# Performance work log

Measured on AMD Instinct MI355X. Metric: run time of the kernel, lower is better.

## Reference

```python
import jax, jax.numpy as jnp
import numpy as np

MODEL_DIM = 512
NUM_HEADS = 8
HEAD_DIM = MODEL_DIM // NUM_HEADS  # 64
NUM_NODE = 1024
CLUSTER = 128
S = 60
EMBED = 0.5


def setup_inputs() -> dict:
    key = jax.random.key(0)
    ks = jax.random.split(key, 16)
    d = MODEL_DIM
    sc = 1.0 / np.sqrt(d)
    inp = {
        "x": jax.random.normal(ks[0], (4, 12, NUM_NODE, d), dtype=jnp.float32),
        "Wq": jax.random.normal(ks[1], (d, d), dtype=jnp.float32) * sc,
        "bq": jnp.zeros((d,), jnp.float32),
        "Wk": jax.random.normal(ks[2], (d, d), dtype=jnp.float32) * sc,
        "bk": jnp.zeros((d,), jnp.float32),
        "Wv": jax.random.normal(ks[3], (d, d), dtype=jnp.float32) * sc,
        "bv": jnp.zeros((d,), jnp.float32),
        "We": jax.random.normal(ks[4], (d, d), dtype=jnp.float32) * sc,
        "be": jnp.zeros((d,), jnp.float32),
        "Wo": jax.random.normal(ks[5], (d, d), dtype=jnp.float32) * sc,
        "bo": jnp.zeros((d,), jnp.float32),
        # adp_pos is initialized to zeros in torch; use small randn for a non-degenerate test
        "adp_pos": jax.random.normal(ks[6], (NUM_NODE, CLUSTER), dtype=jnp.float32) * 0.02,
        "U1": jax.random.normal(ks[7], (HEAD_DIM, S), dtype=jnp.float32) * np.sqrt(2.0 / (HEAD_DIM + S)),
        "U2": jax.random.normal(ks[8], (S, HEAD_DIM), dtype=jnp.float32) * np.sqrt(2.0 / (S + HEAD_DIM)),
    }
    return inp


def _split_heads(t):
    # torch.cat(torch.split(t, head_dim, -1), 0): heads stacked head-major on batch dim
    return jnp.concatenate(jnp.split(t, NUM_HEADS, axis=-1), axis=0)


def _merge_heads(t):
    return jnp.concatenate(jnp.split(t, NUM_HEADS, axis=0), axis=-1)


def _pool_nodes(t):
    # AdaptiveAvgPool2d((CLUSTER, None)) on (B,T,N,D) with N % CLUSTER == 0 -> block mean
    B, T, N, D = t.shape
    return t.reshape(B, T, CLUSTER, N // CLUSTER, D).mean(axis=3)


def reference(x, Wq, bq, Wk, bk, Wv, bv, We, be, Wo, bo, adp_pos, U1, U2):
    q = x @ Wq.T + bq                      # (B,T,N,D)
    k = _pool_nodes(x @ Wk.T + bk)          # (B,T,C,D)
    v = _pool_nodes(x @ Wv.T + bv)          # (B,T,C,D)
    ev = x @ We.T + be                      # (B,T,N,D)

    qh = _split_heads(q)                    # (B*H,T,N,d)
    kh = _split_heads(k)                    # (B*H,T,C,d)
    vh = _split_heads(v)                    # (B*H,T,C,d)
    evh = _split_heads(ev)                  # (B*H,T,N,d)

    # external attention branch: softmax over node dim (-2)
    exa = jax.nn.softmax(evh @ U1, axis=-2)  # (B*H,T,N,S)
    exa_val = (exa @ U2) * EMBED + evh       # (B*H,T,N,d)

    score = jnp.einsum("btnd,btcd->btnc", qh, kh) / np.sqrt(HEAD_DIM)
    score = score + adp_pos[None, None]      # (B*H,T,N,C)
    attn = jax.nn.softmax(score, axis=-1)

    out = attn @ vh + exa_val                # (B*H,T,N,d)
    out = _merge_heads(out)                  # (B,T,N,D)
    return out @ Wo.T + bo
```

## Files before the change

### kernel.cpp

```cpp
#include <hip/hip_runtime.h>


#define LOG2E 1.44269504088896f

typedef __attribute__((ext_vector_type(4))) float f32x4;
typedef __attribute__((ext_vector_type(8))) short bf16x8;

__device__ __forceinline__ unsigned short f2bf(float f) {
    union { float f; unsigned u; } v; v.f = f;
    unsigned r = (v.u + 0x7fffu + ((v.u >> 16) & 1u)) >> 16;
    return (unsigned short)r;
}
__device__ __forceinline__ float bf2f(unsigned short h) {
    union { unsigned u; float f; } v; v.u = ((unsigned)h) << 16;
    return v.f;
}

__global__ void cvt_w(const float* __restrict__ Wq, const float* __restrict__ Wk,
                      const float* __restrict__ Wv, const float* __restrict__ We,
                      const float* __restrict__ Wo, const float* __restrict__ U1,
                      const float* __restrict__ U2,
                      const float* __restrict__ bq, const float* __restrict__ bk,
                      const float* __restrict__ bv, const float* __restrict__ be,
                      unsigned short* __restrict__ Wqe, unsigned short* __restrict__ Wkv,
                      unsigned short* __restrict__ Wob, unsigned short* __restrict__ U1T,
                      unsigned short* __restrict__ U2bT,
                      float* __restrict__ bqe, float* __restrict__ bkv)
{
    int i = blockIdx.x * 256 + threadIdx.x;
    if (i < 524288) {
        int r = i >> 9;
        float v = (r < 512) ? Wq[i] : We[i - 262144];
        Wqe[i] = f2bf(v);
    } else if (i < 1048576) {
        int j = i - 524288; int r = j >> 9;
        float v = (r < 512) ? Wk[j] : Wv[j - 262144];
        Wkv[j] = f2bf(v);
    } else if (i < 1310720) {
        int j = i - 1048576;
        Wob[j] = f2bf(Wo[j]);
    } else if (i < 1314816) {
        int j = i - 1310720; int s = j >> 6, k = j & 63;
        U1T[j] = (s < 60) ? f2bf(U1[k * 60 + s]) : (unsigned short)0;
    } else if (i < 1318912) {
        int j = i - 1314816; int d = j >> 6, s = j & 63;
        U2bT[j] = (s < 60) ? f2bf(U2[s * 64 + d] * 0.5f) : (unsigned short)0;
    } else if (i < 1319936) {
        int j = i - 1318912;
        bqe[j] = (j < 512) ? bq[j] : be[j - 512];
    } else if (i < 1320960) {
        int j = i - 1319936;
        bkv[j] = (j < 512) ? bk[j] : bv[j - 512];
    }
}

__global__ void cvt_pool(const float* __restrict__ x, unsigned short* __restrict__ xb,
                         unsigned short* __restrict__ xpb)
{
    int i = blockIdx.x * 256 + threadIdx.x;
    int d4 = i & 127;
    int btc = i >> 7;
    int bt = btc >> 7, c = btc & 127;
    long base = ((long)(bt * 1024 + c * 8)) * 128 + d4;
    const float4* src = (const float4*)x + base;
    ushort4* dst = (ushort4*)xb + base;
    float sx = 0.f, sy = 0.f, sz = 0.f, sw = 0.f;
#pragma unroll
    for (int j = 0; j < 8; j++) {
        float4 v = src[(long)j * 128];
        sx += v.x; sy += v.y; sz += v.z; sw += v.w;
        ushort4 o;
        o.x = f2bf(v.x); o.y = f2bf(v.y); o.z = f2bf(v.z); o.w = f2bf(v.w);
        dst[(long)j * 128] = o;
    }
    ushort4 p;
    p.x = f2bf(sx * 0.125f); p.y = f2bf(sy * 0.125f);
    p.z = f2bf(sz * 0.125f); p.w = f2bf(sw * 0.125f);
    ((ushort4*)xpb)[(long)btc * 128 + d4] = p;
}

template <int OUTF32>
__global__ __launch_bounds__(256, 2) void gemm_bt(
    const unsigned short* __restrict__ A, const unsigned short* __restrict__ W,
    const float* __restrict__ bias, void* __restrict__ Cout,
    int M, int N, int K)
{
    __shared__ __attribute__((aligned(16))) unsigned short As[128 * 32];
    __shared__ __attribute__((aligned(16))) unsigned short Bs[128 * 32];
    const int tid = threadIdx.x;
    const int wave = tid >> 6, lane = tid & 63;
    const int quad = lane >> 4, l16 = lane & 15;
    const int m0 = blockIdx.x * 128, n0 = blockIdx.y * 128;
    const int wm = (wave & 1) * 64, wn = (wave >> 1) * 64;

    f32x4 acc[4][4];
#pragma unroll
    for (int i = 0; i < 4; i++)
#pragma unroll
        for (int j = 0; j < 4; j++) acc[i][j] = (f32x4){0.f, 0.f, 0.f, 0.f};

    const int c0 = tid, c1 = tid + 256;
    const int r0 = c0 >> 2, kc0 = (c0 & 3) * 8;
    const int r1 = c1 >> 2, kc1 = (c1 & 3) * 8;

    for (int k0 = 0; k0 < K; k0 += 32) {
        int4 a0 = *(const int4*)(A + (long)(m0 + r0) * K + k0 + kc0);
        int4 a1 = *(const int4*)(A + (long)(m0 + r1) * K + k0 + kc1);
        int4 b0 = *(const int4*)(W + (long)(n0 + r0) * K + k0 + kc0);
        int4 b1 = *(const int4*)(W + (long)(n0 + r1) * K + k0 + kc1);
        __syncthreads();
        *(int4*)&As[c0 * 8] = a0; *(int4*)&As[c1 * 8] = a1;
        *(int4*)&Bs[c0 * 8] = b0; *(int4*)&Bs[c1 * 8] = b1;
        __syncthreads();
        bf16x8 af[4], bfr[4];
#pragma unroll
        for (int t = 0; t < 4; t++)
            af[t] = *(const bf16x8*)&As[(wm + t * 16 + l16) * 32 + quad * 8];
#pragma unroll
        for (int t = 0; t < 4; t++)
            bfr[t] = *(const bf16x8*)&Bs[(wn + t * 16 + l16) * 32 + quad * 8];
#pragma unroll
        for (int tm = 0; tm < 4; tm++)
#pragma unroll
            for (int tn = 0; tn < 4; tn++)
                acc[tm][tn] = __builtin_amdgcn_mfma_f32_16x16x32_bf16(
                    af[tm], bfr[tn], acc[tm][tn], 0, 0, 0);
    }

#pragma unroll
    for (int tm = 0; tm < 4; tm++)
#pragma unroll
        for (int tn = 0; tn < 4; tn++) {
            int cc = n0 + wn + tn * 16 + l16;
            float bv = bias[cc];
#pragma unroll
            for (int r = 0; r < 4; r++) {
                int rr = m0 + wm + tm * 16 + quad * 4 + r;
                float v = acc[tm][tn][r] + bv;
                if (OUTF32) ((float*)Cout)[(long)rr * N + cc] = v;
                else        ((unsigned short*)Cout)[(long)rr * N + cc] = f2bf(v);
            }
        }
}

__global__ __launch_bounds__(256, 2) void g2_kv(
    const unsigned short* __restrict__ A, const unsigned short* __restrict__ W,
    const float* __restrict__ bias, unsigned short* __restrict__ kvK,
    unsigned short* __restrict__ vT)
{
    const int M = 6144, N = 1024, K = 512;
    __shared__ __attribute__((aligned(16))) unsigned short As[128 * 32];
    __shared__ __attribute__((aligned(16))) unsigned short Bs[128 * 32];
    const int tid = threadIdx.x;
    const int wave = tid >> 6, lane = tid & 63;
    const int quad = lane >> 4, l16 = lane & 15;
    const int m0 = blockIdx.x * 128, n0 = blockIdx.y * 128;
    const int wm = (wave & 1) * 64, wn = (wave >> 1) * 64;
    (void)M;

    f32x4 acc[4][4];
#pragma unroll
    for (int i = 0; i < 4; i++)
#pragma unroll
        for (int j = 0; j < 4; j++) acc[i][j] = (f32x4){0.f, 0.f, 0.f, 0.f};

    const int c0 = tid, c1 = tid + 256;
    const int r0 = c0 >> 2, kc0 = (c0 & 3) * 8;
    const int r1 = c1 >> 2, kc1 = (c1 & 3) * 8;

    for (int k0 = 0; k0 < K; k0 += 32) {
        int4 a0 = *(const int4*)(A + (long)(m0 + r0) * K + k0 + kc0);
        int4 a1 = *(const int4*)(A + (long)(m0 + r1) * K + k0 + kc1);
        int4 b0 = *(const int4*)(W + (long)(n0 + r0) * K + k0 + kc0);
        int4 b1 = *(const int4*)(W + (long)(n0 + r1) * K + k0 + kc1);
        __syncthreads();
        *(int4*)&As[c0 * 8] = a0; *(int4*)&As[c1 * 8] = a1;
        *(int4*)&Bs[c0 * 8] = b0; *(int4*)&Bs[c1 * 8] = b1;
        __syncthreads();
        bf16x8 af[4], bfr[4];
#pragma unroll
        for (int t = 0; t < 4; t++)
            af[t] = *(const bf16x8*)&As[(wm + t * 16 + l16) * 32 + quad * 8];
#pragma unroll
        for (int t = 0; t < 4; t++)
            bfr[t] = *(const bf16x8*)&Bs[(wn + t * 16 + l16) * 32 + quad * 8];
#pragma unroll
        for (int tm = 0; tm < 4; tm++)
#pragma unroll
            for (int tn = 0; tn < 4; tn++)
                acc[tm][tn] = __builtin_amdgcn_mfma_f32_16x16x32_bf16(
                    af[tm], bfr[tn], acc[tm][tn], 0, 0, 0);
    }

#pragma unroll
    for (int tm = 0; tm < 4; tm++)
#pragma unroll
        for (int tn = 0; tn < 4; tn++) {
            int cc = n0 + wn + tn * 16 + l16;
            float bv = bias[cc];
            int rrb = m0 + wm + tm * 16 + quad * 4;
            if (cc < 512) {
#pragma unroll
                for (int r = 0; r < 4; r++)
                    kvK[(long)(rrb + r) * 512 + cc] = f2bf(acc[tm][tn][r] + bv);
            } else {
                int hh = (cc - 512) >> 6, dd = (cc - 512) & 63;
                int btv = rrb >> 7, cv = rrb & 127;
                ushort4 o;
                o.x = f2bf(acc[tm][tn][0] + bv);
                o.y = f2bf(acc[tm][tn][1] + bv);
                o.z = f2bf(acc[tm][tn][2] + bv);
                o.w = f2bf(acc[tm][tn][3] + bv);
                *(ushort4*)(vT + ((long)(btv * 8 + hh) * 64 + dd) * 128 + cv) = o;
            }
        }
}

__global__ __launch_bounds__(256, 2) void ez_kernel(
    const unsigned short* __restrict__ qev, const unsigned short* __restrict__ U1T,
    unsigned short* __restrict__ Z)
{
    __shared__ __attribute__((aligned(16))) unsigned short evs[128 * 72];
    __shared__ __attribute__((aligned(16))) unsigned short u1s[64 * 72];
    int tid = threadIdx.x, bx = blockIdx.x;
    int bt = bx >> 6, h = (bx >> 3) & 7, nb = bx & 7;
    int wave = tid >> 6, lane = tid & 63, quad = lane >> 4, l16 = lane & 15;

#pragma unroll
    for (int i = 0; i < 4; i++) {
        int c = tid + i * 256; int row = c >> 3, kc = (c & 7) * 8;
        *(int4*)&evs[row * 72 + kc] =
            *(const int4*)(qev + ((long)(bt * 1024 + nb * 128 + row)) * 1024 + 512 + h * 64 + kc);
    }
#pragma unroll
    for (int i = 0; i < 2; i++) {
        int c = tid + i * 256; int row = c >> 3, kc = (c & 7) * 8;
        *(int4*)&u1s[row * 72 + kc] = *(const int4*)(U1T + row * 64 + kc);
    }
    __syncthreads();

    f32x4 acc[2][4];
#pragma unroll
    for (int i = 0; i < 2; i++)
#pragma unroll
        for (int t = 0; t < 4; t++) acc[i][t] = (f32x4){0.f, 0.f, 0.f, 0.f};

#pragma unroll
    for (int kt = 0; kt < 2; kt++) {
        bf16x8 a[2], b[4];
#pragma unroll
        for (int i = 0; i < 2; i++)
            a[i] = *(const bf16x8*)&evs[((wave * 2 + i) * 16 + l16) * 72 + kt * 32 + quad * 8];
#pragma unroll
        for (int t = 0; t < 4; t++)
            b[t] = *(const bf16x8*)&u1s[(t * 16 + l16) * 72 + kt * 32 + quad * 8];
#pragma unroll
        for (int i = 0; i < 2; i++)
#pragma unroll
            for (int t = 0; t < 4; t++)
                acc[i][t] = __builtin_amdgcn_mfma_f32_16x16x32_bf16(a[i], b[t], acc[i][t], 0, 0, 0);
    }

    long zb = (long)(bt * 8 + h) * 1024 + nb * 128;
#pragma unroll
    for (int i = 0; i < 2; i++)
#pragma unroll
        for (int t = 0; t < 4; t++) {
            int s = t * 16 + l16;
            if (s < 60) {
#pragma unroll
                for (int r = 0; r < 4; r++) {
                    int rr = (wave * 2 + i) * 16 + quad * 4 + r;
                    Z[(zb + rr) * 60 + s] = f2bf(acc[i][t][r]);
                }
            }
        }
}

__global__ __launch_bounds__(256, 2) void es_kernel(
    const unsigned short* __restrict__ Z, float* __restrict__ mS, float* __restrict__ lSinv)
{
    __shared__ float ms[4][64];
    __shared__ float ls[4][64];
    int tid = threadIdx.x;
    int s = tid & 63, g = tid >> 6;
    long zb = (long)blockIdx.x * 1024 * 60;
    float m = -1e30f, l = 0.f;
    if (s < 60) {
        for (int r = 0; r < 256; r++) {
            float z = bf2f(Z[zb + (long)(g * 256 + r) * 60 + s]);
            float nm = fmaxf(m, z);
            l = l * exp2f((m - nm) * LOG2E) + exp2f((z - nm) * LOG2E);
            m = nm;
        }
    }
    ms[g][s] = m; ls[g][s] = l;
    __syncthreads();
    if (tid < 60) {
        float M = fmaxf(fmaxf(ms[0][tid], ms[1][tid]), fmaxf(ms[2][tid], ms[3][tid]));
        float L = 0.f;
#pragma unroll
        for (int gg = 0; gg < 4; gg++) L += ls[gg][tid] * exp2f((ms[gg][tid] - M) * LOG2E);
        mS[blockIdx.x * 60 + tid] = M;
        lSinv[blockIdx.x * 60 + tid] = 1.0f / L;
    }
}

__global__ __launch_bounds__(256, 3) void att_kernel(
    const unsigned short* __restrict__ qev, const unsigned short* __restrict__ kvK,
    const unsigned short* __restrict__ vT, const unsigned short* __restrict__ Z,
    const float* __restrict__ mS, const float* __restrict__ lI,
    const float* __restrict__ adp, const unsigned short* __restrict__ U2bT,
    unsigned short* __restrict__ attn_out)
{
    __shared__ __attribute__((aligned(16))) unsigned short Ps[128 * 136];

    int tid = threadIdx.x, bx = blockIdx.x;
    int bt = bx >> 6, h = (bx >> 3) & 7, nb = bx & 7;
    int wave = tid >> 6, lane = tid & 63, quad = lane >> 4, l16 = lane & 15;
    int n0 = nb * 128;
    const int g = bt * 8 + h;
    const long qrow0 = (long)bt * 1024 + n0;

    f32x4 sc[2][8];
#pragma unroll
    for (int i = 0; i < 2; i++)
#pragma unroll
        for (int t = 0; t < 8; t++) sc[i][t] = (f32x4){0.f, 0.f, 0.f, 0.f};

#pragma unroll
    for (int kt = 0; kt < 2; kt++) {
        bf16x8 a[2];
#pragma unroll
        for (int i = 0; i < 2; i++)
            a[i] = *(const bf16x8*)(qev + (qrow0 + (wave * 2 + i) * 16 + l16) * 1024
                                    + h * 64 + kt * 32 + quad * 8);
#pragma unroll
        for (int tn = 0; tn < 8; tn++) {
            bf16x8 b = *(const bf16x8*)(kvK + (long)(bt * 128 + tn * 16 + l16) * 512
                                        + h * 64 + kt * 32 + quad * 8);
#pragma unroll
            for (int i = 0; i < 2; i++)
                sc[i][tn] = __builtin_amdgcn_mfma_f32_16x16x32_bf16(a[i], b, sc[i][tn], 0, 0, 0);
        }
    }

#pragma unroll
    for (int i = 0; i < 2; i++) {
#pragma unroll
        for (int tn = 0; tn < 8; tn++)
#pragma unroll
            for (int r = 0; r < 4; r++) {
                int rr = (wave * 2 + i) * 16 + quad * 4 + r;
                sc[i][tn][r] = sc[i][tn][r] * 0.125f + adp[(n0 + rr) * 128 + tn * 16 + l16];
            }
        float rmax[4], rsum[4];
#pragma unroll
        for (int r = 0; r < 4; r++) {
            float m = sc[i][0][r];
#pragma unroll
            for (int tn = 1; tn < 8; tn++) m = fmaxf(m, sc[i][tn][r]);
#pragma unroll
            for (int d = 1; d < 16; d <<= 1) m = fmaxf(m, __shfl_xor(m, d, 64));
            rmax[r] = m; rsum[r] = 0.f;
        }
#pragma unroll
        for (int tn = 0; tn < 8; tn++)
#pragma unroll
            for (int r = 0; r < 4; r++) {
                float p = exp2f((sc[i][tn][r] - rmax[r]) * LOG2E);
                sc[i][tn][r] = p; rsum[r] += p;
            }
#pragma unroll
        for (int r = 0; r < 4; r++) {
#pragma unroll
            for (int d = 1; d < 16; d <<= 1) rsum[r] += __shfl_xor(rsum[r], d, 64);
            rsum[r] = 1.0f / rsum[r];
        }
#pragma unroll
        for (int tn = 0; tn < 8; tn++)
#pragma unroll
            for (int r = 0; r < 4; r++) {
                int rr = (wave * 2 + i) * 16 + quad * 4 + r;
                Ps[rr * 136 + tn * 16 + l16] = f2bf(sc[i][tn][r] * rsum[r]);
            }
    }

    f32x4 oc[2][4];
#pragma unroll
    for (int i = 0; i < 2; i++)
#pragma unroll
        for (int t = 0; t < 4; t++) oc[i][t] = (f32x4){0.f, 0.f, 0.f, 0.f};

#pragma unroll
    for (int kt = 0; kt < 4; kt++) {
        bf16x8 a[2];
#pragma unroll
        for (int i = 0; i < 2; i++)
            a[i] = *(const bf16x8*)&Ps[((wave * 2 + i) * 16 + l16) * 136 + kt * 32 + quad * 8];
#pragma unroll
        for (int tn = 0; tn < 4; tn++) {
            bf16x8 b = *(const bf16x8*)(vT + ((long)g * 64 + tn * 16 + l16) * 128
                                        + kt * 32 + quad * 8);
#pragma unroll
            for (int i = 0; i < 2; i++)
                oc[i][tn] = __builtin_amdgcn_mfma_f32_16x16x32_bf16(a[i], b, oc[i][tn], 0, 0, 0);
        }
    }

#pragma unroll
    for (int kt = 0; kt < 2; kt++) {
        int sb = kt * 32 + quad * 8;
        float4 ma = *(const float4*)(mS + (long)g * 60 + sb);
        float4 mb2 = *(const float4*)(mS + (long)g * 60 + sb + 4);
        float4 la = *(const float4*)(lI + (long)g * 60 + sb);
        float4 lb2 = *(const float4*)(lI + (long)g * 60 + sb + 4);
        float mv[8] = {ma.x, ma.y, ma.z, ma.w, mb2.x, mb2.y, mb2.z, mb2.w};
        float lv[8] = {la.x, la.y, la.z, la.w, lb2.x, lb2.y, lb2.z, lb2.w};
        bf16x8 ea[2];
#pragma unroll
        for (int i = 0; i < 2; i++) {
            int row = (wave * 2 + i) * 16 + l16;
            const unsigned short* zp = Z + ((long)g * 1024 + n0 + row) * 60 + sb;
            uint2 z0 = *(const uint2*)zp;
            uint2 z1 = *(const uint2*)(zp + 4);
            unsigned zz[4] = {z0.x, z0.y, z1.x, z1.y};
            unsigned short es_[8];
#pragma unroll
            for (int j = 0; j < 8; j++) {
                unsigned short zh = (unsigned short)((zz[j >> 1] >> ((j & 1) * 16)) & 0xffff);
                float e = (sb + j < 60)
                    ? exp2f((bf2f(zh) - mv[j]) * LOG2E) * lv[j] : 0.f;
                es_[j] = f2bf(e);
            }
            ea[i] = *(bf16x8*)es_;
        }
#pragma unroll
        for (int tn = 0; tn < 4; tn++) {
            bf16x8 b = *(const bf16x8*)(U2bT + (tn * 16 + l16) * 64 + sb);
#pragma unroll
            for (int i = 0; i < 2; i++)
                oc[i][tn] = __builtin_amdgcn_mfma_f32_16x16x32_bf16(ea[i], b, oc[i][tn], 0, 0, 0);
        }
    }

#pragma unroll
    for (int i = 0; i < 2; i++)
#pragma unroll
        for (int tn = 0; tn < 4; tn++)
#pragma unroll
            for (int r = 0; r < 4; r++) {
                int rr = (wave * 2 + i) * 16 + quad * 4 + r;
                int cc = tn * 16 + l16;
                float ev = bf2f(qev[(qrow0 + rr) * 1024 + 512 + h * 64 + cc]);
                attn_out[(qrow0 + rr) * 512 + h * 64 + cc] = f2bf(oc[i][tn][r] + ev);
            }
}

extern "C" void kernel_launch(void* const* d_in, const int* in_sizes, int n_in,
                              void* d_out, int out_size, void* d_ws, size_t ws_size,
                              hipStream_t stream)
{
    const float* x   = (const float*)d_in[0];
    const float* Wq  = (const float*)d_in[1];
    const float* bq  = (const float*)d_in[2];
    const float* Wk  = (const float*)d_in[3];
    const float* bk  = (const float*)d_in[4];
    const float* Wv  = (const float*)d_in[5];
    const float* bv  = (const float*)d_in[6];
    const float* We  = (const float*)d_in[7];
    const float* be  = (const float*)d_in[8];
    const float* Wo  = (const float*)d_in[9];
    const float* bo  = (const float*)d_in[10];
    const float* adp = (const float*)d_in[11];
    const float* U1  = (const float*)d_in[12];
    const float* U2  = (const float*)d_in[13];

    char* ws = (char*)d_ws;
    unsigned short* xb   = (unsigned short*)(ws + 0);
    unsigned short* aout = xb;
    unsigned short* xpb  = (unsigned short*)(ws + 50331648);
    unsigned short* qev  = (unsigned short*)(ws + 56623104);
    unsigned short* kvK  = (unsigned short*)(ws + 157286400);
    unsigned short* vT   = (unsigned short*)(ws + 163577856);
    unsigned short* Zb   = (unsigned short*)(ws + 169869312);
    unsigned short* Wqe  = (unsigned short*)(ws + 217055232);
    unsigned short* Wkv  = (unsigned short*)(ws + 218103808);
    unsigned short* Wob  = (unsigned short*)(ws + 219152384);
    unsigned short* U1T  = (unsigned short*)(ws + 219676672);
    unsigned short* U2bT = (unsigned short*)(ws + 219684864);
    float*          mSb  = (float*)(ws + 219693056);
    float*          lIb  = (float*)(ws + 219785216);
    float*          bqe  = (float*)(ws + 219877376);
    float*          bkv  = (float*)(ws + 219881472);

    cvt_w<<<5160, 256, 0, stream>>>(Wq, Wk, Wv, We, Wo, U1, U2, bq, bk, bv, be,
                                    Wqe, Wkv, Wob, U1T, U2bT, bqe, bkv);
    cvt_pool<<<3072, 256, 0, stream>>>(x, xb, xpb);

    gemm_bt<0><<<dim3(384, 8), 256, 0, stream>>>(xb,  Wqe, bqe, (void*)qev, 49152, 1024, 512);
    g2_kv<<<dim3(48, 8), 256, 0, stream>>>(xpb, Wkv, bkv, kvK, vT);

    ez_kernel<<<3072, 256, 0, stream>>>(qev, U1T, Zb);
    es_kernel<<<384, 256, 0, stream>>>(Zb, mSb, lIb);
    att_kernel<<<3072, 256, 0, stream>>>(qev, kvK, vT, Zb, mSb, lIb, adp, U2bT, aout);

    gemm_bt<1><<<dim3(384, 4), 256, 0, stream>>>(aout, Wob, bo, d_out, 49152, 512, 512);
}
```

Measured before the change: 477.9 us.

## Use direct global-to-LDS loads in GEMMs and pre-permute adp_pos for attention

The GEMM kernels now load tiles with global_load_lds straight into shared memory, skipping the round trip through registers, and their occupancy hint goes from 2 to 3 blocks. A new adp_prep kernel rearranges adp_pos into each lane's MFMA fragment order, so att_kernel reads it with contiguous float4 loads instead of scattered scalar loads, and att_kernel's occupancy hint goes from 3 to 4. The costs are an extra small kernel launch per call and register pressure from the tighter launch bounds.

Result: slower. 489.9 us (+2.5%).

```diff
diff --git a/kernel.cpp b/kernel.cpp
--- a/kernel.cpp
+++ b/kernel.cpp
@@ -5,6 +5,11 @@
 
 typedef __attribute__((ext_vector_type(4))) float f32x4;
 typedef __attribute__((ext_vector_type(8))) short bf16x8;
+
+#define GLD16(gptr, ldsptr)                                                     \
+    __builtin_amdgcn_global_load_lds(                                           \
+        (const __attribute__((address_space(1))) unsigned int*)(gptr),          \
+        (__attribute__((address_space(3))) unsigned int*)(ldsptr), 16, 0, 0)
 
 __device__ __forceinline__ unsigned short f2bf(float f) {
     union { float f; unsigned u; } v; v.f = f;
@@ -54,6 +59,19 @@
     }
 }
 
+__global__ void adp_prep(const float* __restrict__ adp, float* __restrict__ adpP)
+{
+    int id = blockIdx.x * 256 + threadIdx.x;
+    int nb = id >> 14;
+    int tid = (id >> 6) & 255;
+    int j = id & 63;
+    int wave = tid >> 6, quad = (tid >> 4) & 3, l16 = tid & 15;
+    int i = j >> 5, tn = (j >> 2) & 7, r = j & 3;
+    int row = nb * 128 + wave * 32 + i * 16 + quad * 4 + r;
+    int col = tn * 16 + l16;
+    adpP[id] = adp[row * 128 + col];
+}
+
 __global__ void cvt_pool(const float* __restrict__ x, unsigned short* __restrict__ xb,
                          unsigned short* __restrict__ xpb)
 {
@@ -80,7 +98,7 @@
 }
 
 template <int OUTF32>
-__global__ __launch_bounds__(256, 2) void gemm_bt(
+__global__ __launch_bounds__(256, 3) void gemm_bt(
     const unsigned short* __restrict__ A, const unsigned short* __restrict__ W,
     const float* __restrict__ bias, void* __restrict__ Cout,
     int M, int N, int K)
@@ -104,13 +122,11 @@
     const int r1 = c1 >> 2, kc1 = (c1 & 3) * 8;
 
     for (int k0 = 0; k0 < K; k0 += 32) {
-        int4 a0 = *(const int4*)(A + (long)(m0 + r0) * K + k0 + kc0);
-        int4 a1 = *(const int4*)(A + (long)(m0 + r1) * K + k0 + kc1);
-        int4 b0 = *(const int4*)(W + (long)(n0 + r0) * K + k0 + kc0);
-        int4 b1 = *(const int4*)(W + (long)(n0 + r1) * K + k0 + kc1);
         __syncthreads();
-        *(int4*)&As[c0 * 8] = a0; *(int4*)&As[c1 * 8] = a1;
-        *(int4*)&Bs[c0 * 8] = b0; *(int4*)&Bs[c1 * 8] = b1;
+        GLD16(A + (long)(m0 + r0) * K + k0 + kc0, &As[c0 * 8]);
+        GLD16(A + (long)(m0 + r1) * K + k0 + kc1, &As[c1 * 8]);
+        GLD16(W + (long)(n0 + r0) * K + k0 + kc0, &Bs[c0 * 8]);
+        GLD16(W + (long)(n0 + r1) * K + k0 + kc1, &Bs[c1 * 8]);
         __syncthreads();
         bf16x8 af[4], bfr[4];
 #pragma unroll
@@ -143,12 +159,12 @@
         }
 }
 
-__global__ __launch_bounds__(256, 2) void g2_kv(
+__global__ __launch_bounds__(256, 3) void g2_kv(
     const unsigned short* __restrict__ A, const unsigned short* __restrict__ W,
     const float* __restrict__ bias, unsigned short* __restrict__ kvK,
     unsigned short* __restrict__ vT)
 {
-    const int M = 6144, N = 1024, K = 512;
+    const int K = 512;
     __shared__ __attribute__((aligned(16))) unsigned short As[128 * 32];
     __shared__ __attribute__((aligned(16))) unsigned short Bs[128 * 32];
     const int tid = threadIdx.x;
@@ -156,7 +172,6 @@
     const int quad = lane >> 4, l16 = lane & 15;
     const int m0 = blockIdx.x * 128, n0 = blockIdx.y * 128;
     const int wm = (wave & 1) * 64, wn = (wave >> 1) * 64;
-    (void)M;
 
     f32x4 acc[4][4];
 #pragma unroll
@@ -169,13 +184,11 @@
     const int r1 = c1 >> 2, kc1 = (c1 & 3) * 8;
 
     for (int k0 = 0; k0 < K; k0 += 32) {
-        int4 a0 = *(const int4*)(A + (long)(m0 + r0) * K + k0 + kc0);
-        int4 a1 = *(const int4*)(A + (long)(m0 + r1) * K + k0 + kc1);
-        int4 b0 = *(const int4*)(W + (long)(n0 + r0) * K + k0 + kc0);
-        int4 b1 = *(const int4*)(W + (long)(n0 + r1) * K + k0 + kc1);
         __syncthreads();
-        *(int4*)&As[c0 * 8] = a0; *(int4*)&As[c1 * 8] = a1;
-        *(int4*)&Bs[c0 * 8] = b0; *(int4*)&Bs[c1 * 8] = b1;
+        GLD16(A + (long)(m0 + r0) * K + k0 + kc0, &As[c0 * 8]);
+        GLD16(A + (long)(m0 + r1) * K + k0 + kc1, &As[c1 * 8]);
+        GLD16(W + (long)(n0 + r0) * K + k0 + kc0, &Bs[c0 * 8]);
+        GLD16(W + (long)(n0 + r1) * K + k0 + kc1, &Bs[c1 * 8]);
         __syncthreads();
         bf16x8 af[4], bfr[4];
 #pragma unroll
@@ -306,11 +319,11 @@
     }
 }
 
-__global__ __launch_bounds__(256, 3) void att_kernel(
+__global__ __launch_bounds__(256, 4) void att_kernel(
     const unsigned short* __restrict__ qev, const unsigned short* __restrict__ kvK,
     const unsigned short* __restrict__ vT, const unsigned short* __restrict__ Z,
     const float* __restrict__ mS, const float* __restrict__ lI,
-    const float* __restrict__ adp, const unsigned short* __restrict__ U2bT,
+    const float* __restrict__ adpP, const unsigned short* __restrict__ U2bT,
     unsigned short* __restrict__ attn_out)
 {
     __shared__ __attribute__((aligned(16))) unsigned short Ps[128 * 136];
@@ -345,15 +358,17 @@
         }
     }
 
+    const float* ap = adpP + ((long)nb * 256 + tid) * 64;
 #pragma unroll
     for (int i = 0; i < 2; i++) {
+        f32x4 av[8];
+#pragma unroll
+        for (int t = 0; t < 8; t++) av[t] = *(const f32x4*)(ap + i * 32 + t * 4);
 #pragma unroll
         for (int tn = 0; tn < 8; tn++)
 #pragma unroll
-            for (int r = 0; r < 4; r++) {
-                int rr = (wave * 2 + i) * 16 + quad * 4 + r;
-                sc[i][tn][r] = sc[i][tn][r] * 0.125f + adp[(n0 + rr) * 128 + tn * 16 + l16];
-            }
+            for (int r = 0; r < 4; r++)
+                sc[i][tn][r] = sc[i][tn][r] * 0.125f + av[tn][r];
         float rmax[4], rsum[4];
 #pragma unroll
         for (int r = 0; r < 4; r++) {
@@ -493,9 +508,11 @@
     float*          lIb  = (float*)(ws + 219785216);
     float*          bqe  = (float*)(ws + 219877376);
     float*          bkv  = (float*)(ws + 219881472);
+    float*          adpP = (float*)(ws + 219885568);
 
     cvt_w<<<5160, 256, 0, stream>>>(Wq, Wk, Wv, We, Wo, U1, U2, bq, bk, bv, be,
                                     Wqe, Wkv, Wob, U1T, U2bT, bqe, bkv);
+    adp_prep<<<512, 256, 0, stream>>>(adp, adpP);
     cvt_pool<<<3072, 256, 0, stream>>>(x, xb, xpb);
 
     gemm_bt<0><<<dim3(384, 8), 256, 0, stream>>>(xb,  Wqe, bqe, (void*)qev, 49152, 1024, 512);
@@ -503,7 +520,7 @@
 
     ez_kernel<<<3072, 256, 0, stream>>>(qev, U1T, Zb);
     es_kernel<<<384, 256, 0, stream>>>(Zb, mSb, lIb);
-    att_kernel<<<3072, 256, 0, stream>>>(qev, kvK, vT, Zb, mSb, lIb, adp, U2bT, aout);
+    att_kernel<<<3072, 256, 0, stream>>>(qev, kvK, vT, Zb, mSb, lIb, adpP, U2bT, aout);
 
     gemm_bt<1><<<dim3(384, 4), 256, 0, stream>>>(aout, Wob, bo, d_out, 49152, 512, 512);
 }
```
